# Kernel optimization log

Measured on AMD Instinct MI355X. Metric: run time of the kernel, lower is better.

## Reference

```python
import jax, jax.numpy as jnp
import numpy as np

B, CIN, COUT, K = 4096, 128, 128, 9  # batch, in_ch, out_ch, board size / n_offsets


def setup_inputs() -> dict:
    key = jax.random.key(0)
    k1, k2, k3 = jax.random.split(key, 3)
    inputs = jax.random.normal(k1, (B, CIN, K, K), dtype=jnp.float32)   # [B, Cin, 9, 9]
    weights = jax.random.normal(k2, (K, COUT, CIN), dtype=jnp.float32)  # per-offset linear
    bias = jax.random.normal(k3, (K, COUT), dtype=jnp.float32)
    return {"inputs": inputs, "weights": weights, "bias": bias}


def reference(inputs, weights, bias):
    # For each vertical offset k (row of the 9x9 board), gather the slice
    # inputs[:, :, k, :] and apply the k-th linear map plus its bias.
    # out[b, k, oc, x] = sum_i W[k, oc, i] * inputs[b, i, k, x] + bias[k, oc]
    out = jnp.einsum('bikx,koi->bkox', inputs, weights)  # [B, 9, Cout, 9]
    out = out + bias[None, :, :, None]
    return out
```

## Files before the change

kernel.cpp:

```cpp
#include <hip/hip_runtime.h>
#include <hip/hip_bf16.h>


#define NB    4096
#define CINC  128
#define COUTC 128
#define NK    9
#define NX    9
#define BT    8
#define NCOL  (BT * NX)
#define LDK   136
#define ROWF  (NK * NX)
#define OUTK  (COUTC * NX)
#define OUTB  (NK * OUTK)
#define KG    3

typedef __attribute__((ext_vector_type(8))) short short8;
typedef __attribute__((ext_vector_type(4))) float floatx4;
typedef __attribute__((ext_vector_type(2))) float floatx2;

struct F4 { float x, y, z, w; };

__device__ __forceinline__ short f2bf(float f) {
    union { float f; unsigned u; } v; v.f = f;
    unsigned r = v.u + 0x7fff + ((v.u >> 16) & 1);
    return (short)(r >> 16);
}
__device__ __forceinline__ unsigned pack2(float lo, float hi) {
    return (unsigned)(unsigned short)f2bf(lo) | ((unsigned)(unsigned short)f2bf(hi) << 16);
}

__global__ __launch_bounds__(512, 4) void GatherVertical_40656160424516_kernel(
    const float* __restrict__ in, const float* __restrict__ w,
    const float* __restrict__ bias, float* __restrict__ out)
{
    __shared__ __align__(16) char smem[NCOL * LDK * 2 + BT * OUTK * 4];
    short* Il = (short*)smem;
    float* Ol = (float*)(smem + NCOL * LDK * 2);

    const int t = threadIdx.x;

    const int j = blockIdx.x;
    const int xcd = j & 7;
    const int slot = j >> 3;
    const int kg = slot % 3;
    const int btg = slot / 3;
    const int btile = btg * 8 + xcd;
    const int b0 = btile * BT;
    const int k0 = kg * KG;

    const int lane = t & 63;
    const int wv = t >> 6;
    const int lc = lane & 15;
    const int quad = lane >> 4;
    const int oc_base = wv * 16;

    const int i0 = lane * 2;
    const float* rowp = in + ((size_t)(b0 + wv) * CINC + i0) * ROWF;

    F4 sa0, sb0, sa1, sb1; float sc0, sc1;
    auto issue_in = [&](int k) {
        const float* p0 = rowp + k * NX;
        const float* p1 = p0 + ROWF;
        sa0 = *(const F4*)p0; sb0 = *(const F4*)(p0 + 4); sc0 = p0[8];
        sa1 = *(const F4*)p1; sb1 = *(const F4*)(p1 + 4); sc1 = p1[8];
    };
    issue_in(k0);

    unsigned* Iw = (unsigned*)Il;
    const int wbase = ((wv * 9) * LDK + i0) >> 1;

    for (int tk = 0; tk < KG; ++tk) {
        const int k = k0 + tk;

        Iw[wbase + 0 * 68] = pack2(sa0.x, sa1.x);
        Iw[wbase + 1 * 68] = pack2(sa0.y, sa1.y);
        Iw[wbase + 2 * 68] = pack2(sa0.z, sa1.z);
        Iw[wbase + 3 * 68] = pack2(sa0.w, sa1.w);
        Iw[wbase + 4 * 68] = pack2(sb0.x, sb1.x);
        Iw[wbase + 5 * 68] = pack2(sb0.y, sb1.y);
        Iw[wbase + 6 * 68] = pack2(sb0.z, sb1.z);
        Iw[wbase + 7 * 68] = pack2(sb0.w, sb1.w);
        Iw[wbase + 8 * 68] = pack2(sc0, sc1);

        asm volatile("s_waitcnt lgkmcnt(0)" ::: "memory");
        __builtin_amdgcn_s_barrier();

        const float* wp = w + k * (COUTC * CINC) + (oc_base + lc) * CINC + quad * 8;
        float4 w0[4], w1[4];
        #pragma unroll
        for (int s = 0; s < 4; ++s) {
            w0[s] = *(const float4*)(wp + s * 32);
            w1[s] = *(const float4*)(wp + s * 32 + 4);
        }
        const float* bp = bias + k * COUTC + oc_base + quad * 4;
        float bsv[4];
        #pragma unroll
        for (int r = 0; r < 4; ++r) bsv[r] = bp[r];
        __builtin_amdgcn_sched_barrier(0);
        if (tk < KG - 1) issue_in(k + 1);
        __builtin_amdgcn_sched_barrier(0);

        short8 afr[4];
        #pragma unroll
        for (int s = 0; s < 4; ++s) {
            short8 a;
            a[0] = f2bf(w0[s].x); a[1] = f2bf(w0[s].y);
            a[2] = f2bf(w0[s].z); a[3] = f2bf(w0[s].w);
            a[4] = f2bf(w1[s].x); a[5] = f2bf(w1[s].y);
            a[6] = f2bf(w1[s].z); a[7] = f2bf(w1[s].w);
            afr[s] = a;
        }

        floatx4 acc[5];
        #pragma unroll
        for (int n = 0; n < 5; ++n) acc[n] = (floatx4){0.f, 0.f, 0.f, 0.f};
        #pragma unroll
        for (int s = 0; s < 4; ++s) {
            const int kof = s * 32 + quad * 8;
            #pragma unroll
            for (int n = 0; n < 5; ++n) {
                const int col = (n < 4) ? (n * 16 + lc) : (64 + (lc & 7));
                short8 bfr = *(const short8*)&Il[col * LDK + kof];
                acc[n] = __builtin_amdgcn_mfma_f32_16x16x32_bf16(afr[s], bfr, acc[n], 0, 0, 0);
            }
        }

        #pragma unroll
        for (int n = 0; n < 4; ++n) {
            int nx = n * 16 + lc;
            int bl = nx / 9;
            int x = nx - bl * 9;
            float* op = Ol + (bl * COUTC + oc_base + quad * 4) * NX + x;
            #pragma unroll
            for (int r = 0; r < 4; ++r) op[r * NX] = acc[n][r] + bsv[r];
        }
        if (lc < 8) {
            int x = lc + 1;
            float* op = Ol + (7 * COUTC + oc_base + quad * 4) * NX + x;
            #pragma unroll
            for (int r = 0; r < 4; ++r) op[r * NX] = acc[4][r] + bsv[r];
        }

        asm volatile("s_waitcnt lgkmcnt(0)" ::: "memory");
        __builtin_amdgcn_s_barrier();

        const float* src = Ol + wv * OUTK;
        float* dst = out + (size_t)(b0 + wv) * OUTB + k * OUTK;
        #pragma unroll
        for (int s = 0; s < 4; ++s) {
            floatx4 v = *(const floatx4*)(src + s * 256 + lane * 4);
            *(floatx4*)(dst + s * 256 + lane * 4) = v;
        }
        floatx2 v2 = *(const floatx2*)(src + 1024 + lane * 2);
        *(floatx2*)(dst + 1024 + lane * 2) = v2;
    }
}

extern "C" void kernel_launch(void* const* d_in, const int* in_sizes, int n_in,
                              void* d_out, int out_size, void* d_ws, size_t ws_size,
                              hipStream_t stream) {
    const float* in  = (const float*)d_in[0];
    const float* w   = (const float*)d_in[1];
    const float* bs  = (const float*)d_in[2];
    float* out = (float*)d_out;
    dim3 grid((NB / BT) * (NK / KG));
    dim3 block(512);
    GatherVertical_40656160424516_kernel<<<grid, block, 0, stream>>>(in, w, bs, out);
}
```

Measured before the change: 344.5 us.

## Halve batch tile, loop all offsets per block, raise occupancy target

Each block now covers 4 batch elements and all 9 vertical offsets, where it previously covered 8 batch elements and a group of 3 offsets. The XCD-aware swizzle of block indices is removed. Input staging is remapped to one row per thread, with 16-bit LDS writes replacing packed 32-bit writes, and output stores are remapped across all threads. The smaller LDS footprint and a launch bound of 8 blocks per SM aim to raise occupancy. In exchange, each block loads the full weight set, and the MFMA N-tiles are underfilled, with 36 columns padded to 48.

```diff
diff --git a/kernel.cpp b/kernel.cpp
--- a/kernel.cpp
+++ b/kernel.cpp
@@ -7,17 +7,15 @@
 #define COUTC 128
 #define NK    9
 #define NX    9
-#define BT    8
+#define BT    4
 #define NCOL  (BT * NX)
 #define LDK   136
 #define ROWF  (NK * NX)
 #define OUTK  (COUTC * NX)
 #define OUTB  (NK * OUTK)
-#define KG    3
 
 typedef __attribute__((ext_vector_type(8))) short short8;
 typedef __attribute__((ext_vector_type(4))) float floatx4;
-typedef __attribute__((ext_vector_type(2))) float floatx2;
 
 struct F4 { float x, y, z, w; };
 
@@ -26,11 +24,8 @@
     unsigned r = v.u + 0x7fff + ((v.u >> 16) & 1);
     return (short)(r >> 16);
 }
-__device__ __forceinline__ unsigned pack2(float lo, float hi) {
-    return (unsigned)(unsigned short)f2bf(lo) | ((unsigned)(unsigned short)f2bf(hi) << 16);
-}
 
-__global__ __launch_bounds__(512, 4) void GatherVertical_40656160424516_kernel(
+__global__ __launch_bounds__(512, 8) void GatherVertical_40656160424516_kernel(
     const float* __restrict__ in, const float* __restrict__ w,
     const float* __restrict__ bias, float* __restrict__ out)
 {
@@ -39,15 +34,7 @@
     float* Ol = (float*)(smem + NCOL * LDK * 2);
 
     const int t = threadIdx.x;
-
-    const int j = blockIdx.x;
-    const int xcd = j & 7;
-    const int slot = j >> 3;
-    const int kg = slot % 3;
-    const int btg = slot / 3;
-    const int btile = btg * 8 + xcd;
-    const int b0 = btile * BT;
-    const int k0 = kg * KG;
+    const int b0 = blockIdx.x * BT;
 
     const int lane = t & 63;
     const int wv = t >> 6;
@@ -55,33 +42,29 @@
     const int quad = lane >> 4;
     const int oc_base = wv * 16;
 
-    const int i0 = lane * 2;
-    const float* rowp = in + ((size_t)(b0 + wv) * CINC + i0) * ROWF;
+    const int i_st = t & 127;
+    const int bl_st = t >> 7;
+    const float* rowp = in + ((size_t)(b0 + bl_st) * CINC + i_st) * ROWF;
 
-    F4 sa0, sb0, sa1, sb1; float sc0, sc1;
+    F4 sa, sb; float sc;
     auto issue_in = [&](int k) {
-        const float* p0 = rowp + k * NX;
-        const float* p1 = p0 + ROWF;
-        sa0 = *(const F4*)p0; sb0 = *(const F4*)(p0 + 4); sc0 = p0[8];
-        sa1 = *(const F4*)p1; sb1 = *(const F4*)(p1 + 4); sc1 = p1[8];
+        const float* p = rowp + k * NX;
+        sa = *(const F4*)p; sb = *(const F4*)(p + 4); sc = p[8];
     };
-    issue_in(k0);
+    issue_in(0);
 
-    unsigned* Iw = (unsigned*)Il;
-    const int wbase = ((wv * 9) * LDK + i0) >> 1;
+    short* Ilb = Il + bl_st * (NX * LDK) + i_st;
 
-    for (int tk = 0; tk < KG; ++tk) {
-        const int k = k0 + tk;
-
-        Iw[wbase + 0 * 68] = pack2(sa0.x, sa1.x);
-        Iw[wbase + 1 * 68] = pack2(sa0.y, sa1.y);
-        Iw[wbase + 2 * 68] = pack2(sa0.z, sa1.z);
-        Iw[wbase + 3 * 68] = pack2(sa0.w, sa1.w);
-        Iw[wbase + 4 * 68] = pack2(sb0.x, sb1.x);
-        Iw[wbase + 5 * 68] = pack2(sb0.y, sb1.y);
-        Iw[wbase + 6 * 68] = pack2(sb0.z, sb1.z);
-        Iw[wbase + 7 * 68] = pack2(sb0.w, sb1.w);
-        Iw[wbase + 8 * 68] = pack2(sc0, sc1);
+    for (int k = 0; k < NK; ++k) {
+        Ilb[0 * LDK] = f2bf(sa.x);
+        Ilb[1 * LDK] = f2bf(sa.y);
+        Ilb[2 * LDK] = f2bf(sa.z);
+        Ilb[3 * LDK] = f2bf(sa.w);
+        Ilb[4 * LDK] = f2bf(sb.x);
+        Ilb[5 * LDK] = f2bf(sb.y);
+        Ilb[6 * LDK] = f2bf(sb.z);
+        Ilb[7 * LDK] = f2bf(sb.w);
+        Ilb[8 * LDK] = f2bf(sc);
 
         asm volatile("s_waitcnt lgkmcnt(0)" ::: "memory");
         __builtin_amdgcn_s_barrier();
@@ -98,7 +81,7 @@
         #pragma unroll
         for (int r = 0; r < 4; ++r) bsv[r] = bp[r];
         __builtin_amdgcn_sched_barrier(0);
-        if (tk < KG - 1) issue_in(k + 1);
+        if (k < NK - 1) issue_in(k + 1);
         __builtin_amdgcn_sched_barrier(0);
 
         short8 afr[4];
@@ -112,22 +95,22 @@
             afr[s] = a;
         }
 
-        floatx4 acc[5];
+        floatx4 acc[3];
         #pragma unroll
-        for (int n = 0; n < 5; ++n) acc[n] = (floatx4){0.f, 0.f, 0.f, 0.f};
+        for (int n = 0; n < 3; ++n) acc[n] = (floatx4){0.f, 0.f, 0.f, 0.f};
         #pragma unroll
         for (int s = 0; s < 4; ++s) {
             const int kof = s * 32 + quad * 8;
             #pragma unroll
-            for (int n = 0; n < 5; ++n) {
-                const int col = (n < 4) ? (n * 16 + lc) : (64 + (lc & 7));
+            for (int n = 0; n < 3; ++n) {
+                const int col = (n < 2) ? (n * 16 + lc) : (32 + (lc & 3));
                 short8 bfr = *(const short8*)&Il[col * LDK + kof];
                 acc[n] = __builtin_amdgcn_mfma_f32_16x16x32_bf16(afr[s], bfr, acc[n], 0, 0, 0);
             }
         }
 
         #pragma unroll
-        for (int n = 0; n < 4; ++n) {
+        for (int n = 0; n < 2; ++n) {
             int nx = n * 16 + lc;
             int bl = nx / 9;
             int x = nx - bl * 9;
@@ -135,25 +118,30 @@
             #pragma unroll
             for (int r = 0; r < 4; ++r) op[r * NX] = acc[n][r] + bsv[r];
         }
-        if (lc < 8) {
-            int x = lc + 1;
-            float* op = Ol + (7 * COUTC + oc_base + quad * 4) * NX + x;
+        if (lc < 4) {
+            float* op = Ol + (3 * COUTC + oc_base + quad * 4) * NX + 5 + lc;
             #pragma unroll
-            for (int r = 0; r < 4; ++r) op[r * NX] = acc[4][r] + bsv[r];
+            for (int r = 0; r < 4; ++r) op[r * NX] = acc[2][r] + bsv[r];
         }
 
         asm volatile("s_waitcnt lgkmcnt(0)" ::: "memory");
         __builtin_amdgcn_s_barrier();
 
-        const float* src = Ol + wv * OUTK;
-        float* dst = out + (size_t)(b0 + wv) * OUTB + k * OUTK;
+        float* dstk = out + (size_t)b0 * OUTB + k * OUTK;
         #pragma unroll
-        for (int s = 0; s < 4; ++s) {
-            floatx4 v = *(const floatx4*)(src + s * 256 + lane * 4);
-            *(floatx4*)(dst + s * 256 + lane * 4) = v;
+        for (int c = 0; c < 2; ++c) {
+            int fo = (c * 512 + t) * 4;
+            int bl = fo / 1152;
+            int rem = fo - bl * 1152;
+            floatx4 v = *(const floatx4*)(Ol + fo);
+            *(floatx4*)(dstk + (size_t)bl * OUTB + rem) = v;
         }
-        floatx2 v2 = *(const floatx2*)(src + 1024 + lane * 2);
-        *(floatx2*)(dst + 1024 + lane * 2) = v2;
+        if (t < 128) {
+            int fo = (1024 + t) * 4;
+            int rem = fo - 3 * 1152;
+            floatx4 v = *(const floatx4*)(Ol + fo);
+            *(floatx4*)(dstk + (size_t)3 * OUTB + rem) = v;
+        }
     }
 }
 
@@ -164,7 +152,7 @@
     const float* w   = (const float*)d_in[1];
     const float* bs  = (const float*)d_in[2];
     float* out = (float*)d_out;
-    dim3 grid((NB / BT) * (NK / KG));
+    dim3 grid(NB / BT);
     dim3 block(512);
     GatherVertical_40656160424516_kernel<<<grid, block, 0, stream>>>(in, w, bs, out);
 }
```

After: 452.3 us. +31.3%, slower.
